# Optimization experiments

Hardware: AMD Instinct MI355X
Metric: run time of the kernel (lower is better)

## Reference

```python
import jax, jax.numpy as jnp
import numpy as np

H = 8
D_MODEL = 1024
DIM_G = 64
WAVE_LEN = 1000.0


def box_relational_embedding(f_g):
    # f_g: [B, N, 4] -> [B, N, N, 64] trigonometric geometry embedding
    B, N, _ = f_g.shape
    x_min, y_min, x_max, y_max = jnp.split(f_g, 4, axis=-1)  # each [B, N, 1]
    cx = (x_min + x_max) * 0.5
    cy = (y_min + y_max) * 0.5
    w = x_max - x_min + 1.0
    h = y_max - y_min + 1.0
    # row i vs column j deltas, normalized by row box size
    dx = jnp.log(jnp.maximum(jnp.abs((cx - cx.reshape(B, 1, N)) / w), 1e-3))
    dy = jnp.log(jnp.maximum(jnp.abs((cy - cy.reshape(B, 1, N)) / h), 1e-3))
    dw = jnp.log(w / w.reshape(B, 1, N))
    dh = jnp.log(h / h.reshape(B, 1, N))
    pos = jnp.stack([dx, dy, dw, dh], axis=-1)  # [B, N, N, 4]
    feat_range = jnp.arange(DIM_G // 8, dtype=jnp.float32) / (DIM_G / 8.0)
    dim_mat = 1.0 / jnp.power(WAVE_LEN, feat_range)  # [8]
    mul = (100.0 * pos)[..., None] * dim_mat  # [B, N, N, 4, 8]
    mul = mul.reshape(B, N, N, DIM_G // 2)
    return jnp.concatenate([jnp.sin(mul), jnp.cos(mul)], axis=-1)  # [B, N, N, 64]


def setup_inputs() -> dict:
    key = jax.random.key(0)
    ks = jax.random.split(key, 12)
    B, N, D = 16, 256, D_MODEL
    q = jax.random.normal(ks[0], (B, N, D), jnp.float32)
    k = jax.random.normal(ks[1], (B, N, D), jnp.float32)
    v = jax.random.normal(ks[2], (B, N, D), jnp.float32)
    # valid boxes: x_max > x_min, y_max > y_min
    xy = jax.random.uniform(ks[3], (B, N, 2), jnp.float32) * 100.0
    wh = jax.random.uniform(ks[4], (B, N, 2), jnp.float32) * 50.0 + 1.0
    input_box = jnp.concatenate([xy, xy + wh], axis=-1)  # [B, N, 4]
    s = 0.02
    Wq = jax.random.normal(ks[5], (D, D), jnp.float32) * s
    Wk = jax.random.normal(ks[6], (D, D), jnp.float32) * s
    Wv = jax.random.normal(ks[7], (D, D), jnp.float32) * s
    Wo = jax.random.normal(ks[8], (D, D), jnp.float32) * s
    bq = jnp.zeros((D,), jnp.float32)
    bk = jnp.zeros((D,), jnp.float32)
    bv = jnp.zeros((D,), jnp.float32)
    bo = jnp.zeros((D,), jnp.float32)
    Wg = jax.random.normal(ks[9], (H, DIM_G), jnp.float32) * 0.1  # stacked per-head Linear(64,1)
    bg = jax.random.normal(ks[10], (H,), jnp.float32) * 0.1
    return {"input_query": q, "input_key": k, "input_value": v, "input_box": input_box,
            "Wq": Wq, "bq": bq, "Wk": Wk, "bk": bk, "Wv": Wv, "bv": bv,
            "Wg": Wg, "bg": bg, "Wo": Wo, "bo": bo}


def reference(input_query, input_key, input_value, input_box,
              Wq, bq, Wk, bk, Wv, bv, Wg, bg, Wo, bo):
    B, N, D = input_query.shape
    d_k = D // H

    def proj(x, W, b):
        return (x @ W + b).reshape(B, N, H, d_k).transpose(0, 2, 1, 3)  # [B,H,N,dk]

    q = proj(input_query, Wq, bq)
    k = proj(input_key, Wk, bk)
    v = proj(input_value, Wv, bv)

    emb = box_relational_embedding(input_box)  # [B, N, N, 64]
    # per-head Linear(64 -> 1), stacked: [B, H, N, N]
    rel_w = jax.nn.relu(jnp.einsum('bmng,hg->bhmn', emb, Wg) + bg[None, :, None, None])

    scores = jnp.einsum('bhqd,bhkd->bhqk', q, k) / np.sqrt(d_k).astype(np.float32)
    logits = jnp.log(jnp.maximum(rel_w, 1e-6)) + scores
    attn = jax.nn.softmax(logits, axis=-1)  # [B, H, N, N]
    out = jnp.einsum('bhqk,bhkd->bhqd', attn, v)
    out = out.transpose(0, 2, 1, 3).reshape(B, N, D)
    return out @ Wo + bo
```

## Files before the change

kernel.cpp:

```cpp
#include <hip/hip_runtime.h>
#include <hip/hip_bf16.h>
#include <math.h>

#define B_  16
#define N_  256
#define D_  1024
#define H_  8
#define DK_ 128

typedef unsigned short u16;
typedef __attribute__((ext_vector_type(8))) short s8v;
typedef __attribute__((ext_vector_type(4))) float f4v;

__device__ __forceinline__ u16 f2b(float x) {
    union { float f; unsigned u; } v; v.f = x;
    unsigned r = v.u + 0x7fffu + ((v.u >> 16) & 1u);
    return (u16)(r >> 16);
}

__device__ __forceinline__ void gload16(void* lds, const void* g) {
    __builtin_amdgcn_global_load_lds(
        (const __attribute__((address_space(1))) void*)g,
        (__attribute__((address_space(3))) void*)lds, 16, 0, 0);
}

__global__ __launch_bounds__(256)
void cvt_kernel(const float* __restrict__ in, u16* __restrict__ out, int n8)
{
    const int i = blockIdx.x * 256 + threadIdx.x;
    if (i >= n8) return;
    const float4 a = ((const float4*)in)[2 * i];
    const float4 b = ((const float4*)in)[2 * i + 1];
    union { u16 s[8]; uint4 v; } o;
    o.s[0] = f2b(a.x); o.s[1] = f2b(a.y); o.s[2] = f2b(a.z); o.s[3] = f2b(a.w);
    o.s[4] = f2b(b.x); o.s[5] = f2b(b.y); o.s[6] = f2b(b.z); o.s[7] = f2b(b.w);
    ((uint4*)out)[i] = o.v;
}

__global__ __launch_bounds__(256)
void cvtT_kernel(const float* __restrict__ W0, const float* __restrict__ W1,
                 const float* __restrict__ W2, const float* __restrict__ W3,
                 u16* __restrict__ out)
{
    const float* W = (blockIdx.z == 0) ? W0 : (blockIdx.z == 1) ? W1 :
                     (blockIdx.z == 2) ? W2 : W3;
    u16* o = out + (size_t)blockIdx.z * (D_ * D_);
    __shared__ float t[32][33];
    const int k0 = blockIdx.x * 32, n0 = blockIdx.y * 32;
    const int c = threadIdx.x & 31, r8 = threadIdx.x >> 5;
#pragma unroll
    for (int rr = 0; rr < 4; ++rr)
        t[r8 + rr * 8][c] = W[(size_t)(k0 + r8 + rr * 8) * D_ + n0 + c];
    __syncthreads();
#pragma unroll
    for (int rr = 0; rr < 4; ++rr)
        o[(size_t)(n0 + r8 + rr * 8) * D_ + k0 + c] = f2b(t[c][r8 + rr * 8]);
}

__global__ __launch_bounds__(256)
void gemm_kernel(const u16* __restrict__ Ab, const u16* __restrict__ Wtb,
                 const float* __restrict__ b0, const float* __restrict__ b1,
                 const float* __restrict__ b2, void* __restrict__ outb, int mode)
{
    __shared__ __align__(16) u16 As[64][32];
    __shared__ __align__(16) u16 Bs[128][32];

    const int z = blockIdx.z;
    const u16* A  = Ab  + (size_t)z * (4096u * 1024u);
    const u16* Wt = Wtb + (size_t)z * (1024u * 1024u);
    const float* bias = (z == 0) ? b0 : (z == 1) ? b1 : b2;

    const int tid  = threadIdx.x;
    const int lane = tid & 63;
    const int w    = tid >> 6;
    const int l15  = lane & 15;
    const int l4   = lane >> 4;
    const int r2   = w >> 1;
    const int c2   = w & 1;
    const int m0   = blockIdx.y * 64;
    const int n0   = blockIdx.x * 128;

    const int arow = w * 16 + (lane >> 2);
    const int acol = (lane & 3) * 8;
    const int brow0 = w * 32 + (lane >> 2);
    const int brow1 = brow0 + 16;

    f4v acc[2][4] = {};

    for (int kt = 0; kt < 32; ++kt) {
        const int k0 = kt * 32;
        __syncthreads();
        gload16(&As[arow][acol],  A  + (size_t)(m0 + arow) * 1024 + k0 + acol);
        gload16(&Bs[brow0][acol], Wt + (size_t)(n0 + brow0) * 1024 + k0 + acol);
        gload16(&Bs[brow1][acol], Wt + (size_t)(n0 + brow1) * 1024 + k0 + acol);
        __syncthreads();

        s8v af[2], bf[4];
#pragma unroll
        for (int mf = 0; mf < 2; ++mf)
            af[mf] = *(const s8v*)&As[r2 * 32 + mf * 16 + l15][l4 * 8];
#pragma unroll
        for (int nf = 0; nf < 4; ++nf)
            bf[nf] = *(const s8v*)&Bs[c2 * 64 + nf * 16 + l15][l4 * 8];
#pragma unroll
        for (int mf = 0; mf < 2; ++mf)
#pragma unroll
            for (int nf = 0; nf < 4; ++nf)
                acc[mf][nf] = __builtin_amdgcn_mfma_f32_16x16x32_bf16(
                    af[mf], bf[nf], acc[mf][nf], 0, 0, 0);
    }

#pragma unroll
    for (int mf = 0; mf < 2; ++mf) {
#pragma unroll
        for (int nf = 0; nf < 4; ++nf) {
            const int n = n0 + c2 * 64 + nf * 16 + l15;
            const float bb = bias[n];
#pragma unroll
            for (int reg = 0; reg < 4; ++reg) {
                const int m = m0 + r2 * 32 + mf * 16 + l4 * 4 + reg;
                const float val = acc[mf][nf][reg] + bb;
                if (mode == 0) {
                    ((float*)outb)[(size_t)m * 1024 + n] = val;
                } else {
                    const int b = m >> 8, tok = m & 255;
                    const int h = n >> 7, d = n & 127;
                    ((u16*)outb)[(size_t)z * (4096u * 1024u) +
                                 (((size_t)b * H_ + h) * N_ + tok) * DK_ + d] = f2b(val);
                }
            }
        }
    }
}

__global__ __launch_bounds__(256)
void boxbias_kernel(const float* __restrict__ fg, const float* __restrict__ Wg,
                    const float* __restrict__ bg, float* __restrict__ lb)
{
    __shared__ float sWg[512];
    __shared__ float sbg[8];
    const int tid = threadIdx.x;
    const int b = blockIdx.x >> 8;
    const int i = blockIdx.x & 255;

    sWg[tid] = Wg[tid];
    sWg[tid + 256] = Wg[tid + 256];
    if (tid < 8) sbg[tid] = bg[tid];

    const float4 bi = *(const float4*)&fg[(size_t)(b * N_ + i) * 4];
    const float cxi = 0.5f * (bi.x + bi.z);
    const float cyi = 0.5f * (bi.y + bi.w);
    const float wi  = bi.z - bi.x + 1.0f;
    const float hi  = bi.w - bi.y + 1.0f;

    const int j = tid;
    const float4 bj = *(const float4*)&fg[(size_t)(b * N_ + j) * 4];
    const float cxj = 0.5f * (bj.x + bj.z);
    const float cyj = 0.5f * (bj.y + bj.w);
    const float wj  = bj.z - bj.x + 1.0f;
    const float hj  = bj.w - bj.y + 1.0f;

    const float pos[4] = {
        logf(fmaxf(fabsf((cxi - cxj) / wi), 1e-3f)) * 100.0f,
        logf(fmaxf(fabsf((cyi - cyj) / hi), 1e-3f)) * 100.0f,
        logf(wi / wj) * 100.0f,
        logf(hi / hj) * 100.0f
    };
    const float dim[8] = {1.0f, 0.421696503f, 0.177827941f, 0.0749894209f,
                          0.0316227766f, 0.0133352143f, 0.00562341325f, 0.00237137371f};

    float sv[32], cv[32];
#pragma unroll
    for (int p = 0; p < 4; ++p)
#pragma unroll
        for (int q = 0; q < 8; ++q)
            __sincosf(pos[p] * dim[q], &sv[p * 8 + q], &cv[p * 8 + q]);

    __syncthreads();
#pragma unroll
    for (int h = 0; h < 8; ++h) {
        float acc = sbg[h];
        const float* wrow = &sWg[h * 64];
#pragma unroll
        for (int g = 0; g < 32; ++g)
            acc = fmaf(sv[g], wrow[g], fmaf(cv[g], wrow[32 + g], acc));
        const float rel = fmaxf(acc, 0.0f);
        lb[(((size_t)b * H_ + h) * N_ + i) * N_ + j] = logf(fmaxf(rel, 1e-6f));
    }
}

__global__ __launch_bounds__(256)
void attn_mfma_kernel(const u16* __restrict__ qp, const u16* __restrict__ kp,
                      const u16* __restrict__ vp, const float* __restrict__ lb,
                      u16* __restrict__ ao)
{
    __shared__ __align__(16) u16 Ks[32][136];
    __shared__ __align__(16) u16 Vt[128][40];
    __shared__ __align__(16) u16 Ps[4][32][40];

    const int tid  = threadIdx.x;
    const int lane = tid & 63;
    const int w    = tid >> 6;
    const int l15  = lane & 15;
    const int l4   = lane >> 4;
    const int bh   = blockIdx.x >> 1;
    const int qt   = blockIdx.x & 1;
    const int q0   = qt * 128 + w * 32;

    s8v qf[2][4];
    const u16* qb = qp + ((size_t)bh * N_ + q0) * DK_;
#pragma unroll
    for (int mf = 0; mf < 2; ++mf)
#pragma unroll
        for (int ks = 0; ks < 4; ++ks)
            qf[mf][ks] = *(const s8v*)(qb + (size_t)(mf * 16 + l15) * DK_ + ks * 32 + l4 * 8);

    f4v o[2][8] = {};
    float m_r[2][4], l_r[2][4];
#pragma unroll
    for (int mf = 0; mf < 2; ++mf)
#pragma unroll
        for (int r = 0; r < 4; ++r) { m_r[mf][r] = -INFINITY; l_r[mf][r] = 0.0f; }

    const float scale = 0.08838834764831845f;
    const float* lbb = lb + ((size_t)bh * N_ + q0) * N_;

    const int sr = tid >> 3;
    const int sc = (tid & 7) * 16;

    for (int kt = 0; kt < 8; ++kt) {
        __syncthreads();
        {
            const u16* ksrc = kp + ((size_t)bh * N_ + kt * 32) * DK_;
            *(s8v*)&Ks[sr][sc]     = *(const s8v*)(ksrc + (size_t)sr * DK_ + sc);
            *(s8v*)&Ks[sr][sc + 8] = *(const s8v*)(ksrc + (size_t)sr * DK_ + sc + 8);
        }
        {
            const u16* vsrc = vp + ((size_t)bh * N_ + kt * 32) * DK_;
            const s8v v0 = *(const s8v*)(vsrc + (size_t)sr * DK_ + sc);
            const s8v v1 = *(const s8v*)(vsrc + (size_t)sr * DK_ + sc + 8);
#pragma unroll
            for (int jj = 0; jj < 8; ++jj) {
                Vt[sc + jj][sr]     = (u16)v0[jj];
                Vt[sc + 8 + jj][sr] = (u16)v1[jj];
            }
        }
        __syncthreads();

        f4v s[2][2] = {};
#pragma unroll
        for (int ks = 0; ks < 4; ++ks) {
#pragma unroll
            for (int kf = 0; kf < 2; ++kf) {
                const s8v kb = *(const s8v*)&Ks[kf * 16 + l15][ks * 32 + l4 * 8];
#pragma unroll
                for (int mf = 0; mf < 2; ++mf)
                    s[mf][kf] = __builtin_amdgcn_mfma_f32_16x16x32_bf16(
                        qf[mf][ks], kb, s[mf][kf], 0, 0, 0);
            }
        }
#pragma unroll
        for (int mf = 0; mf < 2; ++mf)
#pragma unroll
            for (int kf = 0; kf < 2; ++kf)
#pragma unroll
                for (int r = 0; r < 4; ++r)
                    s[mf][kf][r] = fmaf(s[mf][kf][r], scale,
                        lbb[(size_t)(mf * 16 + l4 * 4 + r) * N_ + kt * 32 + kf * 16 + l15]);

#pragma unroll
        for (int mf = 0; mf < 2; ++mf) {
            float rm[4], al[4];
#pragma unroll
            for (int r = 0; r < 4; ++r) rm[r] = fmaxf(s[mf][0][r], s[mf][1][r]);
#pragma unroll
            for (int st = 1; st <= 8; st <<= 1)
#pragma unroll
                for (int r = 0; r < 4; ++r) rm[r] = fmaxf(rm[r], __shfl_xor(rm[r], st));
#pragma unroll
            for (int r = 0; r < 4; ++r) {
                const float mn = fmaxf(m_r[mf][r], rm[r]);
                al[r] = __expf(m_r[mf][r] - mn);
                m_r[mf][r] = mn;
            }
            float p0[4], p1[4], rs[4];
#pragma unroll
            for (int r = 0; r < 4; ++r) {
                p0[r] = __expf(s[mf][0][r] - m_r[mf][r]);
                p1[r] = __expf(s[mf][1][r] - m_r[mf][r]);
                rs[r] = p0[r] + p1[r];
            }
#pragma unroll
            for (int st = 1; st <= 8; st <<= 1)
#pragma unroll
                for (int r = 0; r < 4; ++r) rs[r] += __shfl_xor(rs[r], st);
#pragma unroll
            for (int r = 0; r < 4; ++r) {
                l_r[mf][r] = l_r[mf][r] * al[r] + rs[r];
                Ps[w][mf * 16 + l4 * 4 + r][l15]      = f2b(p0[r]);
                Ps[w][mf * 16 + l4 * 4 + r][16 + l15] = f2b(p1[r]);
            }
#pragma unroll
            for (int nf = 0; nf < 8; ++nf)
#pragma unroll
                for (int r = 0; r < 4; ++r) o[mf][nf][r] *= al[r];
        }

        s8v pa[2];
#pragma unroll
        for (int mf = 0; mf < 2; ++mf)
            pa[mf] = *(const s8v*)&Ps[w][mf * 16 + l15][l4 * 8];
#pragma unroll
        for (int nf = 0; nf < 8; ++nf) {
            const s8v vb = *(const s8v*)&Vt[nf * 16 + l15][l4 * 8];
#pragma unroll
            for (int mf = 0; mf < 2; ++mf)
                o[mf][nf] = __builtin_amdgcn_mfma_f32_16x16x32_bf16(
                    pa[mf], vb, o[mf][nf], 0, 0, 0);
        }
    }

    const int b = bh >> 3, h = bh & 7;
#pragma unroll
    for (int mf = 0; mf < 2; ++mf) {
        float inv[4];
#pragma unroll
        for (int r = 0; r < 4; ++r) inv[r] = 1.0f / l_r[mf][r];
#pragma unroll
        for (int nf = 0; nf < 8; ++nf) {
#pragma unroll
            for (int r = 0; r < 4; ++r) {
                const int tok = q0 + mf * 16 + l4 * 4 + r;
                const int d = nf * 16 + l15;
                ao[(((size_t)b * N_ + tok) * H_ + h) * DK_ + d] = f2b(o[mf][nf][r] * inv[r]);
            }
        }
    }
}

extern "C" void kernel_launch(void* const* d_in, const int* in_sizes, int n_in,
                              void* d_out, int out_size, void* d_ws, size_t ws_size,
                              hipStream_t stream)
{
    const float* xq = (const float*)d_in[0];
    const float* xk = (const float*)d_in[1];
    const float* xv = (const float*)d_in[2];
    const float* fg = (const float*)d_in[3];
    const float* Wq = (const float*)d_in[4];
    const float* bq = (const float*)d_in[5];
    const float* Wk = (const float*)d_in[6];
    const float* bk = (const float*)d_in[7];
    const float* Wv = (const float*)d_in[8];
    const float* bv = (const float*)d_in[9];
    const float* Wg = (const float*)d_in[10];
    const float* bg = (const float*)d_in[11];
    const float* Wo = (const float*)d_in[12];
    const float* bo = (const float*)d_in[13];

    char* w8 = (char*)d_ws;
    u16*   xb  = (u16*)(w8);
    u16*   Wt  = (u16*)(w8 + 25165824);
    u16*   qkv = (u16*)(w8 + 33554432);
    float* lb  = (float*)(w8 + 58720256);
    u16*   ao  = (u16*)(w8 + 92274688);

    const int n8 = (B_ * N_ * D_) / 8;
    cvt_kernel<<<n8 / 256, 256, 0, stream>>>(xq, xb, n8);
    cvt_kernel<<<n8 / 256, 256, 0, stream>>>(xk, xb + 4194304, n8);
    cvt_kernel<<<n8 / 256, 256, 0, stream>>>(xv, xb + 2 * 4194304, n8);
    cvtT_kernel<<<dim3(32, 32, 4), 256, 0, stream>>>(Wq, Wk, Wv, Wo, Wt);

    gemm_kernel<<<dim3(8, 64, 3), 256, 0, stream>>>(xb, Wt, bq, bk, bv, qkv, 1);

    boxbias_kernel<<<B_ * N_, 256, 0, stream>>>(fg, Wg, bg, lb);

    attn_mfma_kernel<<<B_ * H_ * 2, 256, 0, stream>>>(
        qkv, qkv + 4194304, qkv + 2 * 4194304, lb, ao);

    gemm_kernel<<<dim3(8, 64, 1), 256, 0, stream>>>(
        ao, Wt + 3 * 1048576, bo, bo, bo, d_out, 0);
}
```

Measured before the change: 154.6 us.

## Enlarge GEMM tiles to 128x128 with XCD-aware block mapping, merge cvt launches

The GEMM block tile grows from 64x128 to 128x128, so each wave computes 4x4 MFMA fragments instead of 2x4. This doubles the reuse of each loaded B tile and cuts the number of blocks. Blocks are remapped so that neighbouring M tiles land on the same XCD, which should improve L2 sharing. The three fp32-to-bf16 input conversions are merged into one launch, but the QKV GEMM is now split into three separate 256-block launches, giving fewer blocks per launch for latency hiding.

```diff
diff --git a/kernel.cpp b/kernel.cpp
--- a/kernel.cpp
+++ b/kernel.cpp
@@ -25,16 +25,18 @@
 }
 
 __global__ __launch_bounds__(256)
-void cvt_kernel(const float* __restrict__ in, u16* __restrict__ out, int n8)
-{
+void cvt_kernel(const float* __restrict__ x0, const float* __restrict__ x1,
+                const float* __restrict__ x2, u16* __restrict__ out)
+{
+    const float* in = (blockIdx.y == 0) ? x0 : (blockIdx.y == 1) ? x1 : x2;
+    u16* o = out + (size_t)blockIdx.y * 4194304;
     const int i = blockIdx.x * 256 + threadIdx.x;
-    if (i >= n8) return;
     const float4 a = ((const float4*)in)[2 * i];
     const float4 b = ((const float4*)in)[2 * i + 1];
-    union { u16 s[8]; uint4 v; } o;
-    o.s[0] = f2b(a.x); o.s[1] = f2b(a.y); o.s[2] = f2b(a.z); o.s[3] = f2b(a.w);
-    o.s[4] = f2b(b.x); o.s[5] = f2b(b.y); o.s[6] = f2b(b.z); o.s[7] = f2b(b.w);
-    ((uint4*)out)[i] = o.v;
+    union { u16 s[8]; uint4 v; } t;
+    t.s[0] = f2b(a.x); t.s[1] = f2b(a.y); t.s[2] = f2b(a.z); t.s[3] = f2b(a.w);
+    t.s[4] = f2b(b.x); t.s[5] = f2b(b.y); t.s[6] = f2b(b.z); t.s[7] = f2b(b.w);
+    ((uint4*)o)[i] = t.v;
 }
 
 __global__ __launch_bounds__(256)
@@ -58,75 +60,76 @@
 }
 
 __global__ __launch_bounds__(256)
-void gemm_kernel(const u16* __restrict__ Ab, const u16* __restrict__ Wtb,
-                 const float* __restrict__ b0, const float* __restrict__ b1,
-                 const float* __restrict__ b2, void* __restrict__ outb, int mode)
-{
-    __shared__ __align__(16) u16 As[64][32];
+void gemm_kernel(const u16* __restrict__ A, const u16* __restrict__ Wt,
+                 const float* __restrict__ bias, void* __restrict__ outb,
+                 int mode)
+{
+    __shared__ __align__(16) u16 As[128][32];
     __shared__ __align__(16) u16 Bs[128][32];
 
-    const int z = blockIdx.z;
-    const u16* A  = Ab  + (size_t)z * (4096u * 1024u);
-    const u16* Wt = Wtb + (size_t)z * (1024u * 1024u);
-    const float* bias = (z == 0) ? b0 : (z == 1) ? b1 : b2;
+    const int bid = blockIdx.x;
+    const int xcd = bid & 7;
+    const int wic = bid >> 3;
+    const int by  = xcd * 4 + (wic & 3);
+    const int bx  = wic >> 2;
+    const int m0  = by * 128;
+    const int n0  = bx * 128;
 
     const int tid  = threadIdx.x;
     const int lane = tid & 63;
     const int w    = tid >> 6;
     const int l15  = lane & 15;
     const int l4   = lane >> 4;
-    const int r2   = w >> 1;
-    const int c2   = w & 1;
-    const int m0   = blockIdx.y * 64;
-    const int n0   = blockIdx.x * 128;
-
-    const int arow = w * 16 + (lane >> 2);
-    const int acol = (lane & 3) * 8;
-    const int brow0 = w * 32 + (lane >> 2);
-    const int brow1 = brow0 + 16;
-
-    f4v acc[2][4] = {};
+    const int wr   = w >> 1;
+    const int wc   = w & 1;
+
+    const int gr = tid >> 2;
+    const int gc = (tid & 3) * 8;
+    const u16* asrc = A  + (size_t)(m0 + gr) * 1024 + gc;
+    const u16* bsrc = Wt + (size_t)(n0 + gr) * 1024 + gc;
+
+    f4v acc[4][4] = {};
 
     for (int kt = 0; kt < 32; ++kt) {
         const int k0 = kt * 32;
         __syncthreads();
-        gload16(&As[arow][acol],  A  + (size_t)(m0 + arow) * 1024 + k0 + acol);
-        gload16(&Bs[brow0][acol], Wt + (size_t)(n0 + brow0) * 1024 + k0 + acol);
-        gload16(&Bs[brow1][acol], Wt + (size_t)(n0 + brow1) * 1024 + k0 + acol);
+        gload16(&As[gr][gc],      asrc + k0);
+        gload16(&As[64 + gr][gc], asrc + 64 * 1024 + k0);
+        gload16(&Bs[gr][gc],      bsrc + k0);
+        gload16(&Bs[64 + gr][gc], bsrc + 64 * 1024 + k0);
         __syncthreads();
 
-        s8v af[2], bf[4];
-#pragma unroll
-        for (int mf = 0; mf < 2; ++mf)
-            af[mf] = *(const s8v*)&As[r2 * 32 + mf * 16 + l15][l4 * 8];
-#pragma unroll
-        for (int nf = 0; nf < 4; ++nf)
-            bf[nf] = *(const s8v*)&Bs[c2 * 64 + nf * 16 + l15][l4 * 8];
-#pragma unroll
-        for (int mf = 0; mf < 2; ++mf)
-#pragma unroll
-            for (int nf = 0; nf < 4; ++nf)
-                acc[mf][nf] = __builtin_amdgcn_mfma_f32_16x16x32_bf16(
-                    af[mf], bf[nf], acc[mf][nf], 0, 0, 0);
-    }
-
-#pragma unroll
-    for (int mf = 0; mf < 2; ++mf) {
-#pragma unroll
-        for (int nf = 0; nf < 4; ++nf) {
-            const int n = n0 + c2 * 64 + nf * 16 + l15;
-            const float bb = bias[n];
+        s8v af[4], bf[4];
+#pragma unroll
+        for (int i = 0; i < 4; ++i)
+            af[i] = *(const s8v*)&As[wr * 64 + i * 16 + l15][l4 * 8];
+#pragma unroll
+        for (int j = 0; j < 4; ++j)
+            bf[j] = *(const s8v*)&Bs[wc * 64 + j * 16 + l15][l4 * 8];
+#pragma unroll
+        for (int i = 0; i < 4; ++i)
+#pragma unroll
+            for (int j = 0; j < 4; ++j)
+                acc[i][j] = __builtin_amdgcn_mfma_f32_16x16x32_bf16(
+                    af[i], bf[j], acc[i][j], 0, 0, 0);
+    }
+
+#pragma unroll
+    for (int j = 0; j < 4; ++j) {
+        const int n = n0 + wc * 64 + j * 16 + l15;
+        const float bb = bias[n];
+#pragma unroll
+        for (int i = 0; i < 4; ++i) {
 #pragma unroll
             for (int reg = 0; reg < 4; ++reg) {
-                const int m = m0 + r2 * 32 + mf * 16 + l4 * 4 + reg;
-                const float val = acc[mf][nf][reg] + bb;
+                const int m = m0 + wr * 64 + i * 16 + l4 * 4 + reg;
+                const float val = acc[i][j][reg] + bb;
                 if (mode == 0) {
                     ((float*)outb)[(size_t)m * 1024 + n] = val;
                 } else {
                     const int b = m >> 8, tok = m & 255;
                     const int h = n >> 7, d = n & 127;
-                    ((u16*)outb)[(size_t)z * (4096u * 1024u) +
-                                 (((size_t)b * H_ + h) * N_ + tok) * DK_ + d] = f2b(val);
+                    ((u16*)outb)[(((size_t)b * H_ + h) * N_ + tok) * DK_ + d] = f2b(val);
                 }
             }
         }
@@ -364,19 +367,17 @@
     float* lb  = (float*)(w8 + 58720256);
     u16*   ao  = (u16*)(w8 + 92274688);
 
-    const int n8 = (B_ * N_ * D_) / 8;
-    cvt_kernel<<<n8 / 256, 256, 0, stream>>>(xq, xb, n8);
-    cvt_kernel<<<n8 / 256, 256, 0, stream>>>(xk, xb + 4194304, n8);
-    cvt_kernel<<<n8 / 256, 256, 0, stream>>>(xv, xb + 2 * 4194304, n8);
+    cvt_kernel<<<dim3(2048, 3), 256, 0, stream>>>(xq, xk, xv, xb);
     cvtT_kernel<<<dim3(32, 32, 4), 256, 0, stream>>>(Wq, Wk, Wv, Wo, Wt);
 
-    gemm_kernel<<<dim3(8, 64, 3), 256, 0, stream>>>(xb, Wt, bq, bk, bv, qkv, 1);
+    gemm_kernel<<<256, 256, 0, stream>>>(xb,            Wt,            bq, qkv,           1);
+    gemm_kernel<<<256, 256, 0, stream>>>(xb + 4194304,  Wt + 1048576,  bk, qkv + 4194304, 1);
+    gemm_kernel<<<256, 256, 0, stream>>>(xb + 8388608,  Wt + 2097152,  bv, qkv + 8388608, 1);
 
     boxbias_kernel<<<B_ * N_, 256, 0, stream>>>(fg, Wg, bg, lb);
 
     attn_mfma_kernel<<<B_ * H_ * 2, 256, 0, stream>>>(
         qkv, qkv + 4194304, qkv + 2 * 4194304, lb, ao);
 
-    gemm_kernel<<<dim3(8, 64, 1), 256, 0, stream>>>(
-        ao, Wt + 3 * 1048576, bo, bo, bo, d_out, 0);
-}
+    gemm_kernel<<<256, 256, 0, stream>>>(ao, Wt + 3 * 1048576, bo, d_out, 0);
+}
```

New measurement: 171.7 us. +11.1%, slower.
